# Optimization experiments

Measured on AMD Instinct MI355X. Metric: run time of the kernel, lower is better.

The kernel has to match this reference:

```python
import jax, jax.numpy as jnp
import numpy as np

B, V, T = 256, 128000, 16
TOP_K = 100          # min(100, V - n_targets) == 100 since V >> T
TARGET_MARGIN = 1.0
EPS = 1e-8
NEG = -1e30          # sentinel so masked target slots never enter top-k


def setup_inputs() -> dict:
    key = jax.random.key(0)
    k1, k2 = jax.random.split(key)
    # Non-negative sparse activations (SPLADE-style relu output) in [0,1)
    sparse_rep = jax.random.uniform(k1, (B, V), dtype=jnp.float32)
    # Fixed-length padded target id lists (all rows valid -> n_valid = B)
    target_ids = jax.random.randint(k2, (B, T), 0, V).astype(jnp.int64)
    return {"sparse_rep": sparse_rep, "target_ids": target_ids}


def reference(sparse_rep, target_ids):
    # [B, T] gather of target activations (one batched gather, no per-row loop)
    tgt = jnp.take_along_axis(sparse_rep, target_ids, axis=1)
    # -log(a + eps), per-row mean then batch mean == global mean (fixed T)
    target_loss = -jnp.mean(jnp.log(tgt + EPS))
    # hinge margin on target activations
    margin_loss = jnp.mean(jax.nn.relu(TARGET_MARGIN - tgt))
    # mask out target columns per row, then top-k over remaining vocab
    rows = jnp.arange(sparse_rep.shape[0])[:, None]          # [B, 1]
    masked = sparse_rep.at[rows, target_ids].set(NEG)        # [B, V]
    top_vals = jax.lax.top_k(masked, TOP_K)[0]               # [B, TOP_K]
    negative_loss = jnp.mean(top_vals)
    return (target_loss, margin_loss, negative_loss)
```

## Files before the change

### kernel.cpp

```cpp
#include <hip/hip_runtime.h>
#include <cstddef>
#include <cstdint>

#define B_    256
#define V_    128000
#define T_    16
#define TOPK_ 100
#define TPB   1024
#define CAP   4096
#define NF4   (V_ / 4)
#define NHIST 4096

#define SEG    8
#define CAPSEG 512
#define SEGF4  (NF4 / SEG)
#define TPB1   256
#define TPB2   512
#define T0     0.996f

#define FULL_ITERS 15
#define TAIL       (SEGF4 - FULL_ITERS * TPB1)

#define WS_CAND_BYTES ((size_t)B_ * SEG * CAPSEG * sizeof(float))
#define WS_CNT_BYTES  ((size_t)B_ * SEG * sizeof(int))
#define WS_NEED       (WS_CAND_BYTES + WS_CNT_BYTES)

__global__ void zero_out_kernel(float* o) {
    o[0] = 0.f; o[1] = 0.f; o[2] = 0.f;
}

__global__ __launch_bounds__(TPB1) void collect_kernel(
        const float* __restrict__ sparse,
        const int*   __restrict__ tids,
        float*       __restrict__ cand,
        int*         __restrict__ cnt,
        float*       __restrict__ out) {
    __shared__ float s_vals[CAPSEG];
    __shared__ int   s_ids[T_];
    __shared__ int   s_cnt;

    const int gb  = blockIdx.x;
    const int row = gb >> 3;
    const int seg = gb & 7;
    const int tid = threadIdx.x;

    if (gb == 0 && tid < 3) out[tid] = 0.f;

    if (tid < T_) s_ids[tid] = tids[row * T_ + tid];
    if (tid == 0) s_cnt = 0;
    __syncthreads();

    const float4* __restrict__ rp4 =
        (const float4*)(sparse + (size_t)row * V_) + seg * SEGF4;
    const int colbase = (seg * SEGF4) << 2;

    #pragma unroll 5
    for (int it = 0; it < FULL_ITERS; ++it) {
        const int idx = it * TPB1 + tid;
        float4 v = rp4[idx];
        float mx = fmaxf(fmaxf(v.x, v.y), fmaxf(v.z, v.w));
        if (mx >= T0) {
            int col = colbase + (idx << 2);
            float xs[4] = {v.x, v.y, v.z, v.w};
            #pragma unroll
            for (int c = 0; c < 4; ++c) {
                float x = xs[c];
                if (x >= T0) {
                    int cc = col + c;
                    bool is_t = false;
                    #pragma unroll
                    for (int j = 0; j < T_; ++j) is_t |= (cc == s_ids[j]);
                    if (!is_t) {
                        int k = atomicAdd(&s_cnt, 1);
                        if (k < CAPSEG) s_vals[k] = x;
                    }
                }
            }
        }
    }
    if (tid < TAIL) {
        const int idx = FULL_ITERS * TPB1 + tid;
        float4 v = rp4[idx];
        float mx = fmaxf(fmaxf(v.x, v.y), fmaxf(v.z, v.w));
        if (mx >= T0) {
            int col = colbase + (idx << 2);
            float xs[4] = {v.x, v.y, v.z, v.w};
            #pragma unroll
            for (int c = 0; c < 4; ++c) {
                float x = xs[c];
                if (x >= T0) {
                    int cc = col + c;
                    bool is_t = false;
                    #pragma unroll
                    for (int j = 0; j < T_; ++j) is_t |= (cc == s_ids[j]);
                    if (!is_t) {
                        int k = atomicAdd(&s_cnt, 1);
                        if (k < CAPSEG) s_vals[k] = x;
                    }
                }
            }
        }
    }
    __syncthreads();

    int lc = s_cnt;
    int w  = min(lc, CAPSEG);
    float* __restrict__ dst = cand + (size_t)gb * CAPSEG;
    for (int i = tid; i < w; i += TPB1) dst[i] = s_vals[i];
    if (tid == 0) cnt[gb] = lc;
}

__global__ __launch_bounds__(TPB2) void select_kernel(
        const float* __restrict__ sparse,
        const int*   __restrict__ tids,
        const float* __restrict__ cand,
        const int*   __restrict__ cnt,
        float*       __restrict__ out) {
    __shared__ float    s_cand[CAP];
    __shared__ unsigned s_hist[NHIST];
    __shared__ int      s_ids[T_];
    __shared__ int      s_scnt[SEG];
    __shared__ int      s_off[SEG + 1];
    __shared__ int      s_flag;
    __shared__ int      s_cnt2;
    __shared__ int      s_bstar;
    __shared__ float    s_red[128];

    const int row = blockIdx.x;
    const int tid = threadIdx.x;
    const float* __restrict__ rp = sparse + (size_t)row * V_;

    if (tid < T_) s_ids[tid] = tids[row * T_ + tid];
    __syncthreads();

    if (tid < T_) {
        float x  = rp[s_ids[tid]];
        float tl = -logf(x + 1e-8f);
        float ml = fmaxf(1.0f - x, 0.0f);
        #pragma unroll
        for (int off = 8; off > 0; off >>= 1) {
            tl += __shfl_down(tl, off);
            ml += __shfl_down(ml, off);
        }
        if (tid == 0) {
            atomicAdd(out + 0, tl * (1.0f / (B_ * T_)));
            atomicAdd(out + 1, ml * (1.0f / (B_ * T_)));
        }
    }

    if (tid == 0) {
        int acc = 0, bad = 0;
        #pragma unroll
        for (int s = 0; s < SEG; ++s) {
            int c = cnt[row * SEG + s];
            bad |= (c > CAPSEG);
            int cc = min(c, CAPSEG);
            s_scnt[s] = cc;
            s_off[s]  = acc;
            acc += cc;
        }
        s_off[SEG] = acc;
        s_flag = bad || (acc < TOPK_) || (acc > CAP);
    }
    __syncthreads();

    int cntv;
    if (!s_flag) {
        cntv = s_off[SEG];
        const int sg = tid >> 6;
        const int ln = tid & 63;
        const int len = s_scnt[sg];
        const float* __restrict__ src =
            cand + (size_t)(row * SEG + sg) * CAPSEG;
        float* __restrict__ dstp = s_cand + s_off[sg];
        for (int i = ln; i < len; i += 64) dstp[i] = src[i];
        __syncthreads();
    } else {
        for (int i = tid; i < NHIST; i += TPB2) s_hist[i] = 0u;
        if (tid == 0) s_cnt2 = 0;
        __syncthreads();
        const float4* rp4 = (const float4*)rp;
        for (int i = tid; i < NF4; i += TPB2) {
            float4 v = rp4[i];
            float xs[4] = {v.x, v.y, v.z, v.w};
            #pragma unroll
            for (int c = 0; c < 4; ++c) {
                int b = (int)(xs[c] * (float)NHIST);
                b = min(max(b, 0), NHIST - 1);
                atomicAdd(&s_hist[b], 1u);
            }
        }
        __syncthreads();
        if (tid == 0) {
            for (int j = 0; j < T_; ++j) {
                int id = s_ids[j];
                bool dup = false;
                for (int q = 0; q < j; ++q) dup = dup || (s_ids[q] == id);
                if (!dup) {
                    int b = (int)(rp[id] * (float)NHIST);
                    b = min(max(b, 0), NHIST - 1);
                    s_hist[b]--;
                }
            }
            int acc = 0, b = NHIST - 1;
            for (; b >= 0; --b) {
                acc += (int)s_hist[b];
                if (acc >= TOPK_) break;
            }
            s_bstar = max(b, 0);
        }
        __syncthreads();
        int bstar = s_bstar;
        for (int i = tid; i < NF4; i += TPB2) {
            float4 v = rp4[i];
            int col = i << 2;
            float xs[4] = {v.x, v.y, v.z, v.w};
            #pragma unroll
            for (int c = 0; c < 4; ++c) {
                float x = xs[c];
                int b2 = (int)(x * (float)NHIST);
                b2 = min(max(b2, 0), NHIST - 1);
                if (b2 >= bstar) {
                    int cc = col + c;
                    bool is_t = false;
                    #pragma unroll
                    for (int j = 0; j < T_; ++j) is_t |= (cc == s_ids[j]);
                    if (!is_t) {
                        int k = atomicAdd(&s_cnt2, 1);
                        if (k < CAP) s_cand[k] = x;
                    }
                }
            }
        }
        __syncthreads();
        cntv = min(s_cnt2, CAP);
    }

    int n2 = 128;
    while (n2 < cntv) n2 <<= 1;
    for (int i = cntv + tid; i < n2; i += TPB2) s_cand[i] = -1e30f;
    __syncthreads();

    for (int k = 2; k <= n2; k <<= 1) {
        for (int j = k >> 1; j > 0; j >>= 1) {
            for (int i = tid; i < n2; i += TPB2) {
                int p = i ^ j;
                if (p > i) {
                    float a = s_cand[i], b = s_cand[p];
                    bool asc = ((i & k) == 0);
                    if (asc ? (a > b) : (a < b)) {
                        s_cand[i] = b; s_cand[p] = a;
                    }
                }
            }
            __syncthreads();
        }
    }

    if (tid < 128) {
        float v = (tid < TOPK_) ? s_cand[n2 - 1 - tid] : 0.f;
        s_red[tid] = v;
    }
    __syncthreads();
    #pragma unroll
    for (int off = 64; off > 0; off >>= 1) {
        if (tid < off) s_red[tid] += s_red[tid + off];
        __syncthreads();
    }
    if (tid == 0) atomicAdd(out + 2, s_red[0] * (1.0f / (B_ * TOPK_)));
}

__global__ __launch_bounds__(TPB) void row_kernel(
        const float* __restrict__ sparse,
        const int*   __restrict__ tids,
        float*       __restrict__ out) {
    __shared__ float    s_cand[CAP];
    __shared__ unsigned s_hist[NHIST];
    __shared__ int      s_ids[T_];
    __shared__ int      s_cnt;
    __shared__ int      s_bstar;
    __shared__ float    s_red[128];

    const int row = blockIdx.x;
    const int tid = threadIdx.x;
    const float* __restrict__ rp = sparse + (size_t)row * V_;

    if (tid < T_) s_ids[tid] = tids[row * T_ + tid];
    if (tid == 0) s_cnt = 0;
    __syncthreads();

    if (tid < T_) {
        float x  = rp[s_ids[tid]];
        float tl = -logf(x + 1e-8f);
        float ml = fmaxf(1.0f - x, 0.0f);
        #pragma unroll
        for (int off = 8; off > 0; off >>= 1) {
            tl += __shfl_down(tl, off);
            ml += __shfl_down(ml, off);
        }
        if (tid == 0) {
            atomicAdd(out + 0, tl * (1.0f / (B_ * T_)));
            atomicAdd(out + 1, ml * (1.0f / (B_ * T_)));
        }
    }

    const float4* rp4 = (const float4*)rp;
    for (int i = tid; i < NF4; i += TPB) {
        float4 v = rp4[i];
        int col = i << 2;
        float xs[4] = {v.x, v.y, v.z, v.w};
        #pragma unroll
        for (int c = 0; c < 4; ++c) {
            float x = xs[c];
            if (x >= T0) {
                int cc = col + c;
                bool is_t = false;
                #pragma unroll
                for (int j = 0; j < T_; ++j) is_t |= (cc == s_ids[j]);
                if (!is_t) {
                    int k = atomicAdd(&s_cnt, 1);
                    if (k < CAP) s_cand[k] = x;
                }
            }
        }
    }
    __syncthreads();

    int cnt = s_cnt;
    if (cnt < TOPK_ || cnt > CAP) {
        for (int i = tid; i < NHIST; i += TPB) s_hist[i] = 0u;
        __syncthreads();
        for (int i = tid; i < NF4; i += TPB) {
            float4 v = rp4[i];
            float xs[4] = {v.x, v.y, v.z, v.w};
            #pragma unroll
            for (int c = 0; c < 4; ++c) {
                int b = (int)(xs[c] * (float)NHIST);
                b = min(max(b, 0), NHIST - 1);
                atomicAdd(&s_hist[b], 1u);
            }
        }
        __syncthreads();
        if (tid == 0) {
            for (int j = 0; j < T_; ++j) {
                int id = s_ids[j];
                bool dup = false;
                for (int q = 0; q < j; ++q) dup = dup || (s_ids[q] == id);
                if (!dup) {
                    int b = (int)(rp[id] * (float)NHIST);
                    b = min(max(b, 0), NHIST - 1);
                    s_hist[b]--;
                }
            }
            int acc = 0, b = NHIST - 1;
            for (; b >= 0; --b) {
                acc += (int)s_hist[b];
                if (acc >= TOPK_) break;
            }
            s_bstar = max(b, 0);
            s_cnt = 0;
        }
        __syncthreads();
        int bstar = s_bstar;
        for (int i = tid; i < NF4; i += TPB) {
            float4 v = rp4[i];
            int col = i << 2;
            float xs[4] = {v.x, v.y, v.z, v.w};
            #pragma unroll
            for (int c = 0; c < 4; ++c) {
                float x = xs[c];
                int b = (int)(x * (float)NHIST);
                b = min(max(b, 0), NHIST - 1);
                if (b >= bstar) {
                    int cc = col + c;
                    bool is_t = false;
                    #pragma unroll
                    for (int j = 0; j < T_; ++j) is_t |= (cc == s_ids[j]);
                    if (!is_t) {
                        int k = atomicAdd(&s_cnt, 1);
                        if (k < CAP) s_cand[k] = x;
                    }
                }
            }
        }
        __syncthreads();
        cnt = min(s_cnt, CAP);
    }

    int n2 = 128;
    while (n2 < cnt) n2 <<= 1;
    for (int i = cnt + tid; i < n2; i += TPB) s_cand[i] = -1e30f;
    __syncthreads();

    for (int k = 2; k <= n2; k <<= 1) {
        for (int j = k >> 1; j > 0; j >>= 1) {
            for (int i = tid; i < n2; i += TPB) {
                int p = i ^ j;
                if (p > i) {
                    float a = s_cand[i], b = s_cand[p];
                    bool asc = ((i & k) == 0);
                    if (asc ? (a > b) : (a < b)) {
                        s_cand[i] = b; s_cand[p] = a;
                    }
                }
            }
            __syncthreads();
        }
    }

    if (tid < 128) {
        float v = (tid < TOPK_) ? s_cand[n2 - 1 - tid] : 0.f;
        s_red[tid] = v;
    }
    __syncthreads();
    #pragma unroll
    for (int off = 64; off > 0; off >>= 1) {
        if (tid < off) s_red[tid] += s_red[tid + off];
        __syncthreads();
    }
    if (tid == 0) atomicAdd(out + 2, s_red[0] * (1.0f / (B_ * TOPK_)));
}

extern "C" void kernel_launch(void* const* d_in, const int* in_sizes, int n_in,
                              void* d_out, int out_size, void* d_ws, size_t ws_size,
                              hipStream_t stream) {
    const float* sparse = (const float*)d_in[0];
    const int*   tids   = (const int*)d_in[1];
    float*       out    = (float*)d_out;

    if (d_ws != nullptr && ws_size >= WS_NEED) {
        float* cand = (float*)d_ws;
        int*   cnt  = (int*)((char*)d_ws + WS_CAND_BYTES);
        collect_kernel<<<B_ * SEG, TPB1, 0, stream>>>(sparse, tids, cand, cnt, out);
        select_kernel<<<B_, TPB2, 0, stream>>>(sparse, tids, cand, cnt, out);
    } else {
        zero_out_kernel<<<1, 1, 0, stream>>>(out);
        row_kernel<<<B_, TPB, 0, stream>>>(sparse, tids, out);
    }
}
```

Before: 220.6 us.

## Fuse collect and select via last-block-done counter and histogram selection

Merges the two-kernel collect/select pipeline into one kernel. The last of the 8 segment blocks for each row, found through an atomic done counter with threadfences, does the top-k selection. The bitonic sort is replaced by a 1024-bin histogram over the candidates above the threshold, a direct sum of the bins above the cutoff, and a small serial selection inside the boundary bin. Per-segment candidate capacity shrinks from 512 to 128 and a small init kernel zeroes the outputs and counters. This removes a kernel launch boundary and the sort's many barriers, but adds serial single-thread work and a full-row fallback pass when a segment overflows its capacity.

Result: slower. 444.2 us (+101.4%).

```diff
diff --git a/kernel.cpp b/kernel.cpp
--- a/kernel.cpp
+++ b/kernel.cpp
@@ -12,51 +12,166 @@
 #define NHIST 4096
 
 #define SEG    8
-#define CAPSEG 512
+#define CAPSEG 128
 #define SEGF4  (NF4 / SEG)
-#define TPB1   256
-#define TPB2   512
+#define TPBF   256
 #define T0     0.996f
+#define NB     1024
+#define BINCAP 256
 
 #define FULL_ITERS 15
-#define TAIL       (SEGF4 - FULL_ITERS * TPB1)
+#define TAIL       (SEGF4 - FULL_ITERS * TPBF)
 
 #define WS_CAND_BYTES ((size_t)B_ * SEG * CAPSEG * sizeof(float))
 #define WS_CNT_BYTES  ((size_t)B_ * SEG * sizeof(int))
-#define WS_NEED       (WS_CAND_BYTES + WS_CNT_BYTES)
+#define WS_DONE_BYTES ((size_t)B_ * sizeof(int))
+#define WS_NEED       (WS_CAND_BYTES + WS_CNT_BYTES + WS_DONE_BYTES)
 
 __global__ void zero_out_kernel(float* o) {
     o[0] = 0.f; o[1] = 0.f; o[2] = 0.f;
 }
 
-__global__ __launch_bounds__(TPB1) void collect_kernel(
+__global__ void init_kernel(float* out, int* done) {
+    int t = threadIdx.x;
+    if (t < 3) out[t] = 0.f;
+    if (t < B_) done[t] = 0;
+}
+
+__device__ __forceinline__ float block_select_sum(
+        float* s_vals, int acc, float lo, float scale,
+        unsigned* s_hist, unsigned* s_chunk, float* s_bin, float* s_red,
+        int* p_bstar, int* p_above, int* p_bq, int tid) {
+    for (int i = tid; i < NB; i += TPBF) s_hist[i] = 0u;
+    if (tid == 0) *p_bq = 0;
+    __syncthreads();
+
+    for (int i = tid; i < acc; i += TPBF) {
+        int b = (int)((s_vals[i] - lo) * scale);
+        b = min(max(b, 0), NB - 1);
+        atomicAdd(&s_hist[b], 1u);
+    }
+    __syncthreads();
+
+    {
+        int base = tid << 2;
+        s_chunk[tid] = s_hist[base] + s_hist[base + 1] +
+                       s_hist[base + 2] + s_hist[base + 3];
+    }
+    __syncthreads();
+
+    if (tid == 0) {
+        int above = 0, bstar = 0;
+        for (int c = (NB >> 2) - 1; c >= 0; --c) {
+            int s = (int)s_chunk[c];
+            if (above + s >= TOPK_) {
+                for (int b = (c << 2) + 3; b >= (c << 2); --b) {
+                    int cb = (int)s_hist[b];
+                    if (above + cb >= TOPK_) { bstar = b; break; }
+                    above += cb;
+                }
+                *p_bstar = bstar; *p_above = above;
+                break;
+            }
+            above += s;
+        }
+    }
+    __syncthreads();
+
+    const int bstar = *p_bstar;
+    float local = 0.f;
+    for (int i = tid; i < acc; i += TPBF) {
+        float v = s_vals[i];
+        int b = (int)((v - lo) * scale);
+        b = min(max(b, 0), NB - 1);
+        if (b > bstar) {
+            local += v;
+        } else if (b == bstar) {
+            int k = atomicAdd(p_bq, 1);
+            if (k < BINCAP) s_bin[k] = v;
+        }
+    }
+    s_red[tid] = local;
+    __syncthreads();
+    #pragma unroll
+    for (int off = TPBF / 2; off > 0; off >>= 1) {
+        if (tid < off) s_red[tid] += s_red[tid + off];
+        __syncthreads();
+    }
+
+    float sum = 0.f;
+    if (tid == 0) {
+        sum = s_red[0];
+        int q = *p_bq;
+        int m = TOPK_ - *p_above;
+        if (q <= BINCAP) {
+            for (int t = 0; t < m; ++t) {
+                float bv = -1e30f; int bi = 0;
+                for (int i = 0; i < q; ++i)
+                    if (s_bin[i] > bv) { bv = s_bin[i]; bi = i; }
+                sum += bv; s_bin[bi] = -1e30f;
+            }
+        } else {
+            sum = 0.f;
+            for (int t = 0; t < TOPK_; ++t) {
+                float bv = -1e30f; int bi = 0;
+                for (int i = 0; i < acc; ++i)
+                    if (s_vals[i] > bv) { bv = s_vals[i]; bi = i; }
+                sum += bv; s_vals[bi] = -1e30f;
+            }
+        }
+    }
+    return sum;
+}
+
+__global__ __launch_bounds__(TPBF) void fused_kernel(
         const float* __restrict__ sparse,
         const int*   __restrict__ tids,
         float*       __restrict__ cand,
         int*         __restrict__ cnt,
+        int*         __restrict__ done,
         float*       __restrict__ out) {
-    __shared__ float s_vals[CAPSEG];
-    __shared__ int   s_ids[T_];
-    __shared__ int   s_cnt;
+    __shared__ float    s_vals[SEG * CAPSEG];
+    __shared__ unsigned s_hist[NB];
+    __shared__ unsigned s_chunk[NB / 4];
+    __shared__ float    s_bin[BINCAP];
+    __shared__ float    s_red[TPBF];
+    __shared__ int      s_ids[T_];
+    __shared__ int      s_scnt[SEG];
+    __shared__ int      s_soff[SEG + 1];
+    __shared__ int      s_cnt, s_last, s_flag, s_bstar, s_above, s_bq, s_c2;
 
     const int gb  = blockIdx.x;
     const int row = gb >> 3;
     const int seg = gb & 7;
     const int tid = threadIdx.x;
 
-    if (gb == 0 && tid < 3) out[tid] = 0.f;
-
     if (tid < T_) s_ids[tid] = tids[row * T_ + tid];
     if (tid == 0) s_cnt = 0;
     __syncthreads();
 
-    const float4* __restrict__ rp4 =
-        (const float4*)(sparse + (size_t)row * V_) + seg * SEGF4;
+    const float* __restrict__ rp = sparse + (size_t)row * V_;
+
+    if (seg == 0 && tid < T_) {
+        float x  = rp[s_ids[tid]];
+        float tl = -logf(x + 1e-8f);
+        float ml = fmaxf(1.0f - x, 0.0f);
+        #pragma unroll
+        for (int off = 8; off > 0; off >>= 1) {
+            tl += __shfl_down(tl, off);
+            ml += __shfl_down(ml, off);
+        }
+        if (tid == 0) {
+            atomicAdd(out + 0, tl * (1.0f / (B_ * T_)));
+            atomicAdd(out + 1, ml * (1.0f / (B_ * T_)));
+        }
+    }
+
+    const float4* __restrict__ rp4 = (const float4*)rp + seg * SEGF4;
     const int colbase = (seg * SEGF4) << 2;
 
     #pragma unroll 5
     for (int it = 0; it < FULL_ITERS; ++it) {
-        const int idx = it * TPB1 + tid;
+        const int idx = it * TPBF + tid;
         float4 v = rp4[idx];
         float mx = fmaxf(fmaxf(v.x, v.y), fmaxf(v.z, v.w));
         if (mx >= T0) {
@@ -79,7 +194,7 @@
         }
     }
     if (tid < TAIL) {
-        const int idx = FULL_ITERS * TPB1 + tid;
+        const int idx = FULL_ITERS * TPBF + tid;
         float4 v = rp4[idx];
         float mx = fmaxf(fmaxf(v.x, v.y), fmaxf(v.z, v.w));
         if (mx >= T0) {
@@ -103,90 +218,62 @@
     }
     __syncthreads();
 
-    int lc = s_cnt;
-    int w  = min(lc, CAPSEG);
-    float* __restrict__ dst = cand + (size_t)gb * CAPSEG;
-    for (int i = tid; i < w; i += TPB1) dst[i] = s_vals[i];
-    if (tid == 0) cnt[gb] = lc;
-}
-
-__global__ __launch_bounds__(TPB2) void select_kernel(
-        const float* __restrict__ sparse,
-        const int*   __restrict__ tids,
-        const float* __restrict__ cand,
-        const int*   __restrict__ cnt,
-        float*       __restrict__ out) {
-    __shared__ float    s_cand[CAP];
-    __shared__ unsigned s_hist[NHIST];
-    __shared__ int      s_ids[T_];
-    __shared__ int      s_scnt[SEG];
-    __shared__ int      s_off[SEG + 1];
-    __shared__ int      s_flag;
-    __shared__ int      s_cnt2;
-    __shared__ int      s_bstar;
-    __shared__ float    s_red[128];
-
-    const int row = blockIdx.x;
-    const int tid = threadIdx.x;
-    const float* __restrict__ rp = sparse + (size_t)row * V_;
-
-    if (tid < T_) s_ids[tid] = tids[row * T_ + tid];
-    __syncthreads();
-
-    if (tid < T_) {
-        float x  = rp[s_ids[tid]];
-        float tl = -logf(x + 1e-8f);
-        float ml = fmaxf(1.0f - x, 0.0f);
-        #pragma unroll
-        for (int off = 8; off > 0; off >>= 1) {
-            tl += __shfl_down(tl, off);
-            ml += __shfl_down(ml, off);
-        }
-        if (tid == 0) {
-            atomicAdd(out + 0, tl * (1.0f / (B_ * T_)));
-            atomicAdd(out + 1, ml * (1.0f / (B_ * T_)));
-        }
-    }
-
+    {
+        int lc = s_cnt;
+        int w  = min(lc, CAPSEG);
+        float* __restrict__ dst = cand + (size_t)gb * CAPSEG;
+        for (int i = tid; i < w; i += TPBF) dst[i] = s_vals[i];
+        if (tid == 0) cnt[gb] = lc;
+    }
+
+    __threadfence();
+    if (tid == 0) s_last = (atomicAdd(&done[row], 1) == SEG - 1);
+    __syncthreads();
+    if (!s_last) return;
+    __threadfence();
+
+    if (tid < SEG) s_scnt[tid] = cnt[row * SEG + tid];
+    __syncthreads();
     if (tid == 0) {
         int acc = 0, bad = 0;
         #pragma unroll
         for (int s = 0; s < SEG; ++s) {
-            int c = cnt[row * SEG + s];
+            int c = s_scnt[s];
             bad |= (c > CAPSEG);
             int cc = min(c, CAPSEG);
             s_scnt[s] = cc;
-            s_off[s]  = acc;
+            s_soff[s] = acc;
             acc += cc;
         }
-        s_off[SEG] = acc;
-        s_flag = bad || (acc < TOPK_) || (acc > CAP);
-    }
-    __syncthreads();
-
-    int cntv;
+        s_soff[SEG] = acc;
+        s_flag = bad || (acc < TOPK_);
+    }
+    __syncthreads();
+
     if (!s_flag) {
-        cntv = s_off[SEG];
-        const int sg = tid >> 6;
-        const int ln = tid & 63;
-        const int len = s_scnt[sg];
+        const int sg = tid >> 5, ln = tid & 31;
         const float* __restrict__ src =
             cand + (size_t)(row * SEG + sg) * CAPSEG;
-        float* __restrict__ dstp = s_cand + s_off[sg];
-        for (int i = ln; i < len; i += 64) dstp[i] = src[i];
-        __syncthreads();
+        const int off = s_soff[sg], len = s_scnt[sg];
+        for (int i = ln; i < len; i += 32) s_vals[off + i] = src[i];
+        __syncthreads();
+
+        float sum = block_select_sum(s_vals, s_soff[SEG],
+                                     T0, (float)NB / (1.0f - T0),
+                                     s_hist, s_chunk, s_bin, s_red,
+                                     &s_bstar, &s_above, &s_bq, tid);
+        if (tid == 0) atomicAdd(out + 2, sum * (1.0f / (B_ * TOPK_)));
     } else {
-        for (int i = tid; i < NHIST; i += TPB2) s_hist[i] = 0u;
-        if (tid == 0) s_cnt2 = 0;
-        __syncthreads();
-        const float4* rp4 = (const float4*)rp;
-        for (int i = tid; i < NF4; i += TPB2) {
-            float4 v = rp4[i];
+        for (int i = tid; i < NB; i += TPBF) s_hist[i] = 0u;
+        __syncthreads();
+        const float4* __restrict__ rr4 = (const float4*)rp;
+        for (int i = tid; i < NF4; i += TPBF) {
+            float4 v = rr4[i];
             float xs[4] = {v.x, v.y, v.z, v.w};
             #pragma unroll
             for (int c = 0; c < 4; ++c) {
-                int b = (int)(xs[c] * (float)NHIST);
-                b = min(max(b, 0), NHIST - 1);
+                int b = (int)(xs[c] * (float)NB);
+                b = min(max(b, 0), NB - 1);
                 atomicAdd(&s_hist[b], 1u);
             }
         }
@@ -197,77 +284,52 @@
                 bool dup = false;
                 for (int q = 0; q < j; ++q) dup = dup || (s_ids[q] == id);
                 if (!dup) {
-                    int b = (int)(rp[id] * (float)NHIST);
-                    b = min(max(b, 0), NHIST - 1);
+                    int b = (int)(rp[id] * (float)NB);
+                    b = min(max(b, 0), NB - 1);
                     s_hist[b]--;
                 }
             }
-            int acc = 0, b = NHIST - 1;
+            int above = 0, b = NB - 1;
             for (; b >= 0; --b) {
-                acc += (int)s_hist[b];
-                if (acc >= TOPK_) break;
+                int cb = (int)s_hist[b];
+                if (above + cb >= TOPK_) break;
+                above += cb;
             }
             s_bstar = max(b, 0);
-        }
-        __syncthreads();
-        int bstar = s_bstar;
-        for (int i = tid; i < NF4; i += TPB2) {
-            float4 v = rp4[i];
+            s_c2 = 0;
+        }
+        __syncthreads();
+        const int b1 = s_bstar;
+        const float lo = (float)b1 / (float)NB;
+        for (int i = tid; i < NF4; i += TPBF) {
+            float4 v = rr4[i];
             int col = i << 2;
             float xs[4] = {v.x, v.y, v.z, v.w};
             #pragma unroll
             for (int c = 0; c < 4; ++c) {
                 float x = xs[c];
-                int b2 = (int)(x * (float)NHIST);
-                b2 = min(max(b2, 0), NHIST - 1);
-                if (b2 >= bstar) {
+                int b = (int)(x * (float)NB);
+                b = min(max(b, 0), NB - 1);
+                if (b >= b1) {
                     int cc = col + c;
                     bool is_t = false;
                     #pragma unroll
                     for (int j = 0; j < T_; ++j) is_t |= (cc == s_ids[j]);
                     if (!is_t) {
-                        int k = atomicAdd(&s_cnt2, 1);
-                        if (k < CAP) s_cand[k] = x;
+                        int k = atomicAdd(&s_c2, 1);
+                        if (k < SEG * CAPSEG) s_vals[k] = x;
                     }
                 }
             }
         }
         __syncthreads();
-        cntv = min(s_cnt2, CAP);
-    }
-
-    int n2 = 128;
-    while (n2 < cntv) n2 <<= 1;
-    for (int i = cntv + tid; i < n2; i += TPB2) s_cand[i] = -1e30f;
-    __syncthreads();
-
-    for (int k = 2; k <= n2; k <<= 1) {
-        for (int j = k >> 1; j > 0; j >>= 1) {
-            for (int i = tid; i < n2; i += TPB2) {
-                int p = i ^ j;
-                if (p > i) {
-                    float a = s_cand[i], b = s_cand[p];
-                    bool asc = ((i & k) == 0);
-                    if (asc ? (a > b) : (a < b)) {
-                        s_cand[i] = b; s_cand[p] = a;
-                    }
-                }
-            }
-            __syncthreads();
-        }
-    }
-
-    if (tid < 128) {
-        float v = (tid < TOPK_) ? s_cand[n2 - 1 - tid] : 0.f;
-        s_red[tid] = v;
-    }
-    __syncthreads();
-    #pragma unroll
-    for (int off = 64; off > 0; off >>= 1) {
-        if (tid < off) s_red[tid] += s_red[tid + off];
-        __syncthreads();
-    }
-    if (tid == 0) atomicAdd(out + 2, s_red[0] * (1.0f / (B_ * TOPK_)));
+        int c2 = min(s_c2, SEG * CAPSEG);
+        float sum = block_select_sum(s_vals, c2,
+                                     lo, (float)NB / (1.0f - lo),
+                                     s_hist, s_chunk, s_bin, s_red,
+                                     &s_bstar, &s_above, &s_bq, tid);
+        if (tid == 0) atomicAdd(out + 2, sum * (1.0f / (B_ * TOPK_)));
+    }
 }
 
 __global__ __launch_bounds__(TPB) void row_kernel(
@@ -431,8 +493,9 @@
     if (d_ws != nullptr && ws_size >= WS_NEED) {
         float* cand = (float*)d_ws;
         int*   cnt  = (int*)((char*)d_ws + WS_CAND_BYTES);
-        collect_kernel<<<B_ * SEG, TPB1, 0, stream>>>(sparse, tids, cand, cnt, out);
-        select_kernel<<<B_, TPB2, 0, stream>>>(sparse, tids, cand, cnt, out);
+        int*   done = (int*)((char*)d_ws + WS_CAND_BYTES + WS_CNT_BYTES);
+        init_kernel<<<1, 256, 0, stream>>>(out, done);
+        fused_kernel<<<B_ * SEG, TPBF, 0, stream>>>(sparse, tids, cand, cnt, done, out);
     } else {
         zero_out_kernel<<<1, 1, 0, stream>>>(out);
         row_kernel<<<B_, TPB, 0, stream>>>(sparse, tids, out);
```
